# Kernel tuning notes

Measured on AMD Instinct MI355X. Metric: run time of the kernel, lower is better.

Reference implementation:

```python
import jax, jax.numpy as jnp
import numpy as np

WRAP_PARAM = 1.0  # wrap_param from __init__
MU0 = 0.1         # initial mu baked into the fixed system matrix A at init time


def _diff_matrix(k):
    """Finite-difference matrix: rows 0..k-2 give x[i+1]-x[i]; last row x[-1]-x[-2]."""
    m = -np.eye(k) + np.eye(k, k, 1)
    m[-1, -1] = 1.0
    m[-1, -2] = -1.0
    return m.astype(np.float32)


def _wrap(x, wrap_param=WRAP_PARAM):
    # Robust2DUnwrap.wrap with normalize=False
    return (x + wrap_param) % (2.0 * wrap_param) - wrap_param


def setup_inputs() -> dict:
    key = jax.random.key(0)
    M = N = 112
    b, c = 1, 1
    x = jax.random.normal(key, (b, c, M, N), dtype=jnp.float32) * 2.0
    DM = _diff_matrix(M)
    DN = _diff_matrix(N)
    # A = A1^T A1 + A2^T A2 + mu0*I with A1 = kron(I_N, D_M), A2 = kron(D_N, I_M)
    # (column-major vec convention), equal to kron(I, DM^T DM) + kron(DN^T DN, I) + mu0 I.
    L_M = DM.T @ DM
    L_N = DN.T @ DN
    A = (np.kron(np.eye(N, dtype=np.float32), L_M)
         + np.kron(L_N, np.eye(M, dtype=np.float32))
         + MU0 * np.eye(M * N, dtype=np.float32))
    mu = jnp.array([MU0], dtype=jnp.float32)  # learnable regularization weight
    return {"x": x, "mu": mu, "A": jnp.asarray(A),
            "DM": jnp.asarray(DM), "DN": jnp.asarray(DN)}


def _forward(x, mu, A, DM, DN):
    b, c, M, N = x.shape
    # The torch code computes the wrapped finite differences from a detached copy of x;
    # only the mu*x term carries gradient w.r.t. x.
    xd = jax.lax.stop_gradient(x)
    # d1y = wrap(D_M @ X): vertical differences
    dy = _wrap(jnp.einsum('im,bcmn->bcin', DM, xd))
    dx = _wrap(jnp.einsum('bcmn,jn->bcmj', xd, DN))
    r = jnp.einsum('mi,bcmn->bcin', DM, dy) + jnp.einsum('bcmj,jn->bcmn', dx, DN)
    rhs = r + mu[0] * x
    # column-major (Fortran) vectorization per image -> RHS of shape (M*N, b*c)
    v = jnp.swapaxes(rhs, -1, -2).reshape(b * c, M * N).T
    sol = jnp.linalg.solve(A, v)  # dense (MN)x(MN) solve
    # column-major un-vectorization back to (b, c, M, N)
    return jnp.swapaxes(sol.T.reshape(b, c, N, M), -1, -2)


def reference(x, mu, A, DM, DN):
    return _forward(x, mu, A, DM, DN)
```

## Files before the change

### kernel.cpp

```cpp
#include <hip/hip_runtime.h>
#include <math.h>

#define K 112
#define W 8
#define OWN 14
#define GH 22
#define EXTR 58
#define NSTEN 22
#define NT 512
#define TR 2
#define TC 7
#define NRT 29
#define NCT 16
#define LDPX 116
#define LDP 113
#define MU0A 0.1f

__device__ __forceinline__ float wrapf(float v) {
    return v - 2.0f * floorf(0.5f * v + 0.5f);
}
__device__ __forceinline__ float dcoef(int i) {
    return (i == 0) ? 1.0f : ((i == K - 2) ? 3.0f : 2.0f);
}
__device__ __forceinline__ float ecoef(int i) {
    return (i == K - 2) ? -2.0f : -1.0f;
}

__global__ __launch_bounds__(NT, 1)
void robust2d_cheb8(const float* __restrict__ x_in,
                    const float* __restrict__ mu_in,
                    float* __restrict__ out) {
    __shared__ __align__(16) float xs[60 * LDPX];
    __shared__ float dbufA[EXTR * LDP];
    __shared__ float dbufB[EXTR * LDP];

    const int wg    = blockIdx.x;
    const int ebase = OWN * wg - GH;
    const int tid = threadIdx.x;
    const int ri  = tid >> 4;
    const int ci  = tid & 15;
    const bool act = (ri < NRT);
    const int e0  = act ? (TR * ri) : 0;
    const int j0  = TC * ci;
    const float mu = mu_in[0];

    for (int e = tid; e < 60 * 28; e += NT) {
        int row = e / 28, q = (e % 28) * 4;
        int g = ebase - 1 + row;
        g = min(max(g, 0), K - 1);
        *(float4*)&xs[row * LDPX + q] = *(const float4*)(x_in + g * K + q);
    }
    __syncthreads();

#define XSG(g, j) xs[((g) - ebase + 1) * LDPX + (j)]

    const float theta = 5.1f, delta = 5.0f;
    const float sg = theta / delta;
    float rho = 1.0f / sg;

    float rr[TR][TC], dd[TR][TC], xa[TR][TC];
    float cdg[TR][TC], cvu[TR], cvd[TR], chl[TC], chr[TC];
    #pragma unroll
    for (int c = 0; c < TC; ++c) {
        const int j = j0 + c;
        chl[c] = (j > 0)     ? ecoef(j - 1) : 0.0f;
        chr[c] = (j < K - 1) ? ecoef(j)     : 0.0f;
    }
    #pragma unroll
    for (int r = 0; r < TR; ++r) {
        const int g = ebase + e0 + r;
        const bool alive = act && (g >= 0) && (g < K);
        cvu[r] = (alive && g > 0)     ? ecoef(g - 1) : 0.0f;
        cvd[r] = (alive && g < K - 1) ? ecoef(g)     : 0.0f;
        #pragma unroll
        for (int c = 0; c < TC; ++c) {
            const int j = j0 + c;
            float b = 0.0f;
            if (alive) {
                float vert, horz;
                if (g == 0) {
                    vert = -wrapf(XSG(1, j) - XSG(0, j));
                } else if (g < K - 2) {
                    vert = wrapf(XSG(g, j) - XSG(g - 1, j)) - wrapf(XSG(g + 1, j) - XSG(g, j));
                } else if (g == K - 2) {
                    vert = wrapf(XSG(K - 2, j) - XSG(K - 3, j)) - 2.0f * wrapf(XSG(K - 1, j) - XSG(K - 2, j));
                } else {
                    vert = 2.0f * wrapf(XSG(K - 1, j) - XSG(K - 2, j));
                }
                if (j == 0) {
                    horz = -wrapf(XSG(g, 1) - XSG(g, 0));
                } else if (j < K - 2) {
                    horz = wrapf(XSG(g, j) - XSG(g, j - 1)) - wrapf(XSG(g, j + 1) - XSG(g, j));
                } else if (j == K - 2) {
                    horz = wrapf(XSG(g, K - 2) - XSG(g, K - 3)) - 2.0f * wrapf(XSG(g, K - 1) - XSG(g, K - 2));
                } else {
                    horz = 2.0f * wrapf(XSG(g, K - 1) - XSG(g, K - 2));
                }
                b = vert + horz + mu * XSG(g, j);
            }
            rr[r][c]  = b;
            dd[r][c]  = b * (1.0f / theta);
            xa[r][c]  = dd[r][c];
            cdg[r][c] = alive ? (dcoef(g) + dcoef(j) + MU0A) : 0.0f;
        }
    }

    const int eu = (e0 > 0)        ? (e0 - 1) : 0;
    const int ed = (e0 + 2 < EXTR) ? (e0 + 2) : (EXTR - 1);
    const int jl = (j0 > 0)        ? (j0 - 1) : 0;
    const int jr = (j0 + TC < K)   ? (j0 + TC) : (K - 1);

    float* cur = dbufA;
    float* nxt = dbufB;
    if (act) {
        #pragma unroll
        for (int r = 0; r < TR; ++r)
            #pragma unroll
            for (int c = 0; c < TC; ++c)
                cur[(e0 + r) * LDP + j0 + c] = dd[r][c];
    }
    __syncthreads();

    for (int it = 0; it < NSTEN; ++it) {
        const float rho_n = 1.0f / (2.0f * sg - rho);
        const float ak = rho_n * rho;
        const float bk = 2.0f * rho_n / delta;
        rho = rho_n;

        if (act) {
            float up[TC], dn[TC], lf[TR], rt[TR];
            #pragma unroll
            for (int c = 0; c < TC; ++c) up[c] = cur[eu * LDP + j0 + c];
            #pragma unroll
            for (int c = 0; c < TC; ++c) dn[c] = cur[ed * LDP + j0 + c];
            #pragma unroll
            for (int r = 0; r < TR; ++r) lf[r] = cur[(e0 + r) * LDP + jl];
            #pragma unroll
            for (int r = 0; r < TR; ++r) rt[r] = cur[(e0 + r) * LDP + jr];

            float ap[TR][TC];
            #pragma unroll
            for (int r = 0; r < TR; ++r) {
                #pragma unroll
                for (int c = 0; c < TC; ++c) {
                    float a = cdg[r][c] * dd[r][c];
                    a += cvu[r] * ((r == 0) ? up[c] : dd[0][c]);
                    a += cvd[r] * ((r == 1) ? dn[c] : dd[1][c]);
                    a += chl[c] * ((c == 0)      ? lf[r] : dd[r][c - 1]);
                    a += chr[c] * ((c == TC - 1) ? rt[r] : dd[r][c + 1]);
                    ap[r][c] = a;
                }
            }
            #pragma unroll
            for (int r = 0; r < TR; ++r) {
                #pragma unroll
                for (int c = 0; c < TC; ++c) {
                    const float rv = rr[r][c] - ap[r][c];
                    rr[r][c] = rv;
                    const float dv = ak * dd[r][c] + bk * rv;
                    dd[r][c] = dv;
                    xa[r][c] += dv;
                }
            }
        }

        if (it != NSTEN - 1) {
            if (act) {
                #pragma unroll
                for (int r = 0; r < TR; ++r)
                    #pragma unroll
                    for (int c = 0; c < TC; ++c)
                        nxt[(e0 + r) * LDP + j0 + c] = dd[r][c];
            }
            __syncthreads();
            float* t = cur; cur = nxt; nxt = t;
        }
    }

    if (act && ri >= 11 && ri < 18) {
        #pragma unroll
        for (int r = 0; r < TR; ++r) {
            const int g = ebase + e0 + r;
            #pragma unroll
            for (int c = 0; c < TC; ++c)
                out[g * K + j0 + c] = xa[r][c];
        }
    }
}

extern "C" void kernel_launch(void* const* d_in, const int* in_sizes, int n_in,
                              void* d_out, int out_size, void* d_ws, size_t ws_size,
                              hipStream_t stream) {
    const float* x  = (const float*)d_in[0];
    const float* mu = (const float*)d_in[1];
    float* out = (float*)d_out;
    robust2d_cheb8<<<W, NT, 0, stream>>>(x, mu, out);
}
```

Measured before the change: 28.59 us.

## Load input stencil directly into registers and cut one Chebyshev iteration

Drops the shared-memory staging of the input tile and has each thread read its 4x9 neighbourhood straight from global memory into registers, removing one barrier and the LDS fill. The Chebyshev iteration count drops by one and the halo shrinks to match, so the block needs 448 threads with no idle rows. Fewer iterations cut the number of barrier-separated steps but may reduce solution accuracy. The register-resident stencil raises register use per thread.

```diff
diff --git a/kernel.cpp b/kernel.cpp
--- a/kernel.cpp
+++ b/kernel.cpp
@@ -4,15 +4,12 @@
 #define K 112
 #define W 8
 #define OWN 14
-#define GH 22
-#define EXTR 58
-#define NSTEN 22
-#define NT 512
+#define GH 21
+#define EXTR 56
+#define NSTEN 21
+#define NT 448
 #define TR 2
 #define TC 7
-#define NRT 29
-#define NCT 16
-#define LDPX 116
 #define LDP 113
 #define MU0A 0.1f
 
@@ -27,10 +24,9 @@
 }
 
 __global__ __launch_bounds__(NT, 1)
-void robust2d_cheb8(const float* __restrict__ x_in,
-                    const float* __restrict__ mu_in,
-                    float* __restrict__ out) {
-    __shared__ __align__(16) float xs[60 * LDPX];
+void robust2d_cheb8d(const float* __restrict__ x_in,
+                     const float* __restrict__ mu_in,
+                     float* __restrict__ out) {
     __shared__ float dbufA[EXTR * LDP];
     __shared__ float dbufB[EXTR * LDP];
 
@@ -39,20 +35,22 @@
     const int tid = threadIdx.x;
     const int ri  = tid >> 4;
     const int ci  = tid & 15;
-    const bool act = (ri < NRT);
-    const int e0  = act ? (TR * ri) : 0;
+    const int e0  = TR * ri;
+    const int g0  = ebase + e0;
     const int j0  = TC * ci;
     const float mu = mu_in[0];
 
-    for (int e = tid; e < 60 * 28; e += NT) {
-        int row = e / 28, q = (e % 28) * 4;
-        int g = ebase - 1 + row;
-        g = min(max(g, 0), K - 1);
-        *(float4*)&xs[row * LDPX + q] = *(const float4*)(x_in + g * K + q);
+    float xr[4][9];
+    #pragma unroll
+    for (int dr = 0; dr < 4; ++dr) {
+        const int gr = min(max(g0 - 1 + dr, 0), K - 1);
+        #pragma unroll
+        for (int dc = 0; dc < 9; ++dc) {
+            const int jc = min(max(j0 - 1 + dc, 0), K - 1);
+            xr[dr][dc] = x_in[gr * K + jc];
+        }
     }
-    __syncthreads();
-
-#define XSG(g, j) xs[((g) - ebase + 1) * LDPX + (j)]
+#define XR(gg, jj) xr[(gg) - (g0 - 1)][(jj) - (j0 - 1)]
 
     const float theta = 5.1f, delta = 5.0f;
     const float sg = theta / delta;
@@ -68,8 +66,8 @@
     }
     #pragma unroll
     for (int r = 0; r < TR; ++r) {
-        const int g = ebase + e0 + r;
-        const bool alive = act && (g >= 0) && (g < K);
+        const int g = g0 + r;
+        const bool alive = (g >= 0) && (g < K);
         cvu[r] = (alive && g > 0)     ? ecoef(g - 1) : 0.0f;
         cvd[r] = (alive && g < K - 1) ? ecoef(g)     : 0.0f;
         #pragma unroll
@@ -79,24 +77,24 @@
             if (alive) {
                 float vert, horz;
                 if (g == 0) {
-                    vert = -wrapf(XSG(1, j) - XSG(0, j));
+                    vert = -wrapf(XR(g + 1, j) - XR(g, j));
                 } else if (g < K - 2) {
-                    vert = wrapf(XSG(g, j) - XSG(g - 1, j)) - wrapf(XSG(g + 1, j) - XSG(g, j));
+                    vert = wrapf(XR(g, j) - XR(g - 1, j)) - wrapf(XR(g + 1, j) - XR(g, j));
                 } else if (g == K - 2) {
-                    vert = wrapf(XSG(K - 2, j) - XSG(K - 3, j)) - 2.0f * wrapf(XSG(K - 1, j) - XSG(K - 2, j));
+                    vert = wrapf(XR(g, j) - XR(g - 1, j)) - 2.0f * wrapf(XR(g + 1, j) - XR(g, j));
                 } else {
-                    vert = 2.0f * wrapf(XSG(K - 1, j) - XSG(K - 2, j));
+                    vert = 2.0f * wrapf(XR(g, j) - XR(g - 1, j));
                 }
                 if (j == 0) {
-                    horz = -wrapf(XSG(g, 1) - XSG(g, 0));
+                    horz = -wrapf(XR(g, j + 1) - XR(g, j));
                 } else if (j < K - 2) {
-                    horz = wrapf(XSG(g, j) - XSG(g, j - 1)) - wrapf(XSG(g, j + 1) - XSG(g, j));
+                    horz = wrapf(XR(g, j) - XR(g, j - 1)) - wrapf(XR(g, j + 1) - XR(g, j));
                 } else if (j == K - 2) {
-                    horz = wrapf(XSG(g, K - 2) - XSG(g, K - 3)) - 2.0f * wrapf(XSG(g, K - 1) - XSG(g, K - 2));
+                    horz = wrapf(XR(g, j) - XR(g, j - 1)) - 2.0f * wrapf(XR(g, j + 1) - XR(g, j));
                 } else {
-                    horz = 2.0f * wrapf(XSG(g, K - 1) - XSG(g, K - 2));
+                    horz = 2.0f * wrapf(XR(g, j) - XR(g, j - 1));
                 }
-                b = vert + horz + mu * XSG(g, j);
+                b = vert + horz + mu * XR(g, j);
             }
             rr[r][c]  = b;
             dd[r][c]  = b * (1.0f / theta);
@@ -112,13 +110,11 @@
 
     float* cur = dbufA;
     float* nxt = dbufB;
-    if (act) {
+    #pragma unroll
+    for (int r = 0; r < TR; ++r)
         #pragma unroll
-        for (int r = 0; r < TR; ++r)
-            #pragma unroll
-            for (int c = 0; c < TC; ++c)
-                cur[(e0 + r) * LDP + j0 + c] = dd[r][c];
-    }
+        for (int c = 0; c < TC; ++c)
+            cur[(e0 + r) * LDP + j0 + c] = dd[r][c];
     __syncthreads();
 
     for (int it = 0; it < NSTEN; ++it) {
@@ -127,60 +123,56 @@
         const float bk = 2.0f * rho_n / delta;
         rho = rho_n;
 
-        if (act) {
-            float up[TC], dn[TC], lf[TR], rt[TR];
+        float up[TC], dn[TC], lf[TR], rt[TR];
+        #pragma unroll
+        for (int c = 0; c < TC; ++c) up[c] = cur[eu * LDP + j0 + c];
+        #pragma unroll
+        for (int c = 0; c < TC; ++c) dn[c] = cur[ed * LDP + j0 + c];
+        #pragma unroll
+        for (int r = 0; r < TR; ++r) lf[r] = cur[(e0 + r) * LDP + jl];
+        #pragma unroll
+        for (int r = 0; r < TR; ++r) rt[r] = cur[(e0 + r) * LDP + jr];
+
+        float ap[TR][TC];
+        #pragma unroll
+        for (int r = 0; r < TR; ++r) {
             #pragma unroll
-            for (int c = 0; c < TC; ++c) up[c] = cur[eu * LDP + j0 + c];
+            for (int c = 0; c < TC; ++c) {
+                float a = cdg[r][c] * dd[r][c];
+                a += cvu[r] * ((r == 0) ? up[c] : dd[0][c]);
+                a += cvd[r] * ((r == 1) ? dn[c] : dd[1][c]);
+                a += chl[c] * ((c == 0)      ? lf[r] : dd[r][c - 1]);
+                a += chr[c] * ((c == TC - 1) ? rt[r] : dd[r][c + 1]);
+                ap[r][c] = a;
+            }
+        }
+        #pragma unroll
+        for (int r = 0; r < TR; ++r) {
             #pragma unroll
-            for (int c = 0; c < TC; ++c) dn[c] = cur[ed * LDP + j0 + c];
-            #pragma unroll
-            for (int r = 0; r < TR; ++r) lf[r] = cur[(e0 + r) * LDP + jl];
-            #pragma unroll
-            for (int r = 0; r < TR; ++r) rt[r] = cur[(e0 + r) * LDP + jr];
-
-            float ap[TR][TC];
-            #pragma unroll
-            for (int r = 0; r < TR; ++r) {
-                #pragma unroll
-                for (int c = 0; c < TC; ++c) {
-                    float a = cdg[r][c] * dd[r][c];
-                    a += cvu[r] * ((r == 0) ? up[c] : dd[0][c]);
-                    a += cvd[r] * ((r == 1) ? dn[c] : dd[1][c]);
-                    a += chl[c] * ((c == 0)      ? lf[r] : dd[r][c - 1]);
-                    a += chr[c] * ((c == TC - 1) ? rt[r] : dd[r][c + 1]);
-                    ap[r][c] = a;
-                }
-            }
-            #pragma unroll
-            for (int r = 0; r < TR; ++r) {
-                #pragma unroll
-                for (int c = 0; c < TC; ++c) {
-                    const float rv = rr[r][c] - ap[r][c];
-                    rr[r][c] = rv;
-                    const float dv = ak * dd[r][c] + bk * rv;
-                    dd[r][c] = dv;
-                    xa[r][c] += dv;
-                }
+            for (int c = 0; c < TC; ++c) {
+                const float rv = rr[r][c] - ap[r][c];
+                rr[r][c] = rv;
+                const float dv = ak * dd[r][c] + bk * rv;
+                dd[r][c] = dv;
+                xa[r][c] += dv;
             }
         }
 
         if (it != NSTEN - 1) {
-            if (act) {
+            #pragma unroll
+            for (int r = 0; r < TR; ++r)
                 #pragma unroll
-                for (int r = 0; r < TR; ++r)
-                    #pragma unroll
-                    for (int c = 0; c < TC; ++c)
-                        nxt[(e0 + r) * LDP + j0 + c] = dd[r][c];
-            }
+                for (int c = 0; c < TC; ++c)
+                    nxt[(e0 + r) * LDP + j0 + c] = dd[r][c];
             __syncthreads();
             float* t = cur; cur = nxt; nxt = t;
         }
     }
 
-    if (act && ri >= 11 && ri < 18) {
-        #pragma unroll
-        for (int r = 0; r < TR; ++r) {
-            const int g = ebase + e0 + r;
+    #pragma unroll
+    for (int r = 0; r < TR; ++r) {
+        const int g = g0 + r;
+        if (g >= OWN * wg && g < OWN * wg + OWN) {
             #pragma unroll
             for (int c = 0; c < TC; ++c)
                 out[g * K + j0 + c] = xa[r][c];
@@ -194,5 +186,5 @@
     const float* x  = (const float*)d_in[0];
     const float* mu = (const float*)d_in[1];
     float* out = (float*)d_out;
-    robust2d_cheb8<<<W, NT, 0, stream>>>(x, mu, out);
+    robust2d_cheb8d<<<W, NT, 0, stream>>>(x, mu, out);
 }
```

Result: slower. 29.62 us (+3.6%).
